# Optimization experiments

Measured on AMD Instinct MI355X. Metric: run time of the kernel, lower is better.

The kernel has to match this reference:

```python
import jax, jax.numpy as jnp
import numpy as np
from jax import lax

B, C, HW = 256, 3, 128
OC, K = 16, 3
NH, FANIN, NO = 256, 512, 10
F = OC * 63 * 63  # 63504 flattened features after conv(k=3,valid)->pool(2)


def setup_inputs() -> dict:
    key = jax.random.key(0)
    ks = jax.random.split(key, 8)
    inputs = jax.random.normal(ks[0], (B, C, HW, HW), dtype=jnp.float32)
    conv_w = jax.random.normal(ks[1], (OC, C, K, K), dtype=jnp.float32) * 0.1
    conv_b = jax.random.normal(ks[2], (OC,), dtype=jnp.float32) * 0.1
    hidden_idx = jax.random.randint(ks[3], (NH, FANIN), 0, F, dtype=jnp.int64 if jax.config.jax_enable_x64 else jnp.int32)
    hidden_w = jax.random.normal(ks[4], (NH, FANIN), dtype=jnp.float32) * (1.0 / np.sqrt(FANIN))
    hidden_b = jax.random.normal(ks[5], (NH,), dtype=jnp.float32) * 0.1
    out_w = jax.random.normal(ks[6], (NO, NH), dtype=jnp.float32) * (1.0 / np.sqrt(NH))
    out_b = jax.random.normal(ks[7], (NO,), dtype=jnp.float32) * 0.1
    return {"inputs": inputs, "conv_w": conv_w, "conv_b": conv_b,
            "hidden_idx": hidden_idx, "hidden_w": hidden_w, "hidden_b": hidden_b,
            "out_w": out_w, "out_b": out_b}


def reference(inputs, conv_w, conv_b, hidden_idx, hidden_w, hidden_b, out_w, out_b):
    # --- feature extraction: conv(valid) -> relu -> maxpool(2) -> flatten ---
    x = lax.conv_general_dilated(inputs, conv_w, window_strides=(1, 1), padding='VALID',
                                 dimension_numbers=('NCHW', 'OIHW', 'NCHW'))
    x = jax.nn.relu(x + conv_b[None, :, None, None])            # [B, OC, 126, 126]
    x = lax.reduce_window(x, -jnp.inf, lax.max,
                          window_dimensions=(1, 1, 2, 2),
                          window_strides=(1, 1, 2, 2), padding='VALID')  # [B, OC, 63, 63]
    feats = x.reshape(x.shape[0], -1)                           # [B, F] (row-major == torch.flatten)
    # --- NEAT-style classification: per-node gather -> tiny linear -> sigmoid ---
    gathered = feats[:, hidden_idx]                             # [B, NH, FANIN] irregular gather
    hidden = jax.nn.sigmoid(jnp.einsum('bhk,hk->bh', gathered, hidden_w) + hidden_b)  # [B, NH]
    out = jax.nn.sigmoid(hidden @ out_w.T + out_b)              # [B, NO]
    return out
```

## Files before the change

### kernel.cpp

```cpp
#include <hip/hip_runtime.h>
#include <hip/hip_fp16.h>
#include <math.h>

#define BATCH 256
#define CIN 3
#define HW 128
#define OC 16
#define POOLED 63
#define FEAT 63504
#define NH 256
#define FANIN 512
#define NO 10

#define PADX 134
#define ROWS 12

typedef _Float16 h4 __attribute__((ext_vector_type(4)));
typedef _Float16 h2v __attribute__((ext_vector_type(2)));
typedef float    f4 __attribute__((ext_vector_type(4)));

__global__ __launch_bounds__(256) void conv_pool_kernel(const float* __restrict__ inp,
                                                        const float* __restrict__ cw,
                                                        const float* __restrict__ cb,
                                                        __half* __restrict__ featsT) {
    __shared__ _Float16 sB[ROWS * 16 * PADX];
    const int t    = threadIdx.x;
    const int l    = t & 63;
    const int w    = t >> 6;
    const int q    = l >> 4;
    const int bcol = l & 15;

    const int id = blockIdx.x;
    const int u  = id & 7;
    const int v  = id >> 3;
    const int i  = v >> 1;
    const int g  = 2 * u + (v & 1);
    const int y0 = 2 * i;

#pragma unroll
    for (int bb = 0; bb < 4; ++bb) {
        const int b_l = w * 4 + bb;
#pragma unroll
        for (int rr = 0; rr < 12; ++rr) {
            const int c  = rr >> 2;
            const int dy = rr & 3;
            const float2 vv = *(const float2*)
                &inp[((size_t)(g * 16 + b_l) * CIN + c) * (HW * HW) + (y0 + dy) * HW + 2 * l];
            *(__half2*)&sB[(size_t)((c * 4 + dy) * 16 + b_l) * PADX + 2 * l] =
                __float22half2_rn(vv);
        }
    }
    __syncthreads();

    h4  aF[3][2];
    int bOff[3][2];
    float bias[4];
#pragma unroll
    for (int s = 0; s < 3; ++s) {
        const int rIdx = s * 4 + q;
        const int c    = (rIdx * 11) >> 5;
        const int ky   = rIdx - 3 * c;
        const bool valid = (c < 3);
        float wv[3];
#pragma unroll
        for (int kx = 0; kx < 3; ++kx)
            wv[kx] = valid ? cw[(bcol * CIN + c) * 9 + ky * 3 + kx] : 0.0f;
        aF[s][0][0] = (_Float16)wv[0]; aF[s][0][1] = (_Float16)wv[1];
        aF[s][0][2] = (_Float16)wv[2]; aF[s][0][3] = (_Float16)0.0f;
        aF[s][1][0] = (_Float16)0.0f;  aF[s][1][1] = (_Float16)wv[0];
        aF[s][1][2] = (_Float16)wv[1]; aF[s][1][3] = (_Float16)wv[2];
#pragma unroll
        for (int ys = 0; ys < 2; ++ys) {
            const int row = valid ? (c * 4 + ys + ky) : ys;
            bOff[s][ys] = (row * 16 + bcol) * PADX;
        }
    }
#pragma unroll
    for (int r = 0; r < 4; ++r) bias[r] = cb[4 * q + r];

    const int jend = (16 * w + 16 < 63) ? (16 * w + 16) : 63;
    for (int j = 16 * w; j < jend; ++j) {
        f4 d00 = {0.f,0.f,0.f,0.f}, d01 = d00, d10 = d00, d11 = d00;
#pragma unroll
        for (int s = 0; s < 3; ++s) {
            const _Float16* p0 = &sB[bOff[s][0] + 2 * j];
            const _Float16* p1 = &sB[bOff[s][1] + 2 * j];
            const h2v a0 = *(const h2v*)p0, a1 = *(const h2v*)(p0 + 2);
            const h2v c0 = *(const h2v*)p1, c1 = *(const h2v*)(p1 + 2);
            const h4 bF0 = {a0[0], a0[1], a1[0], a1[1]};
            const h4 bF1 = {c0[0], c0[1], c1[0], c1[1]};
            d00 = __builtin_amdgcn_mfma_f32_16x16x16f16(aF[s][0], bF0, d00, 0, 0, 0);
            d01 = __builtin_amdgcn_mfma_f32_16x16x16f16(aF[s][1], bF0, d01, 0, 0, 0);
            d10 = __builtin_amdgcn_mfma_f32_16x16x16f16(aF[s][0], bF1, d10, 0, 0, 0);
            d11 = __builtin_amdgcn_mfma_f32_16x16x16f16(aF[s][1], bF1, d11, 0, 0, 0);
        }
#pragma unroll
        for (int r = 0; r < 4; ++r) {
            const float mv = fmaxf(fmaxf(d00[r], d01[r]), fmaxf(d10[r], d11[r]));
            const float rv = fmaxf(mv + bias[r], 0.0f);
            const int oc = 4 * q + r;
            featsT[(size_t)(oc * 3969 + i * POOLED + j) * BATCH + g * 16 + bcol] =
                __float2half_rn(rv);
        }
    }
}

__global__ __launch_bounds__(256) void hidden_kernel(const __half* __restrict__ featsT,
                                                     const int* __restrict__ hidx,
                                                     const float* __restrict__ hw,
                                                     float* __restrict__ hiddenP) {
    __shared__ int   sidx[128];
    __shared__ float swt[128];
    __shared__ float red[4][256];
    const int h = blockIdx.x;
    const int q = blockIdx.y;
    const int t = threadIdx.x;
    if (t < 128) {
        sidx[t] = hidx[h * FANIN + q * 128 + t];
        swt[t]  = hw[h * FANIN + q * 128 + t];
    }
    __syncthreads();

    const int l   = t & 63;
    const int w   = t >> 6;
    const int hl  = l & 31;
    const int sel = l >> 5;
    float acc[8] = {0.f,0.f,0.f,0.f,0.f,0.f,0.f,0.f};
#pragma unroll
    for (int m = 0; m < 16; ++m) {
        const int kloc = w * 32 + 2 * m + sel;
        const uint4 v = *(const uint4*)(featsT + (size_t)sidx[kloc] * BATCH + 8 * hl);
        const __half2* hp = reinterpret_cast<const __half2*>(&v);
        const float wt = swt[kloc];
#pragma unroll
        for (int d2 = 0; d2 < 4; ++d2) {
            const float2 f = __half22float2(hp[d2]);
            acc[2 * d2 + 0] += f.x * wt;
            acc[2 * d2 + 1] += f.y * wt;
        }
    }
#pragma unroll
    for (int e = 0; e < 8; ++e) acc[e] += __shfl_xor(acc[e], 32);
    if (sel == 0) {
#pragma unroll
        for (int e = 0; e < 8; ++e) red[w][8 * hl + e] = acc[e];
    }
    __syncthreads();

    if (t < 256) {
        const float s = red[0][t] + red[1][t] + red[2][t] + red[3][t];
        hiddenP[((size_t)q * NH + h) * BATCH + t] = s;
    }
}

__global__ __launch_bounds__(256) void out_kernel(const float* __restrict__ hiddenP,
                                                  const float* __restrict__ hb,
                                                  const float* __restrict__ ow,
                                                  const float* __restrict__ ob,
                                                  float* __restrict__ out) {
    __shared__ float red[256];
    const int o  = blockIdx.x;
    const int bt = blockIdx.y;
    const int tb = threadIdx.x & 15;
    const int hg = threadIdx.x >> 4;
    const int b  = bt * 16 + tb;
    float acc = 0.f;
#pragma unroll
    for (int k = 0; k < 16; ++k) {
        const int h = hg * 16 + k;
        const float s = hiddenP[(0 * NH + h) * BATCH + b]
                      + hiddenP[(1 * NH + h) * BATCH + b]
                      + hiddenP[(2 * NH + h) * BATCH + b]
                      + hiddenP[(3 * NH + h) * BATCH + b] + hb[h];
        const float hs = 1.0f / (1.0f + __expf(-s));
        acc += hs * ow[o * NH + h];
    }
    red[threadIdx.x] = acc;
    __syncthreads();
    if (hg == 0) {
        float s = 0.f;
#pragma unroll
        for (int gg = 0; gg < 16; ++gg) s += red[gg * 16 + tb];
        out[b * NO + o] = 1.0f / (1.0f + __expf(-(s + ob[o])));
    }
}

extern "C" void kernel_launch(void* const* d_in, const int* in_sizes, int n_in,
                              void* d_out, int out_size, void* d_ws, size_t ws_size,
                              hipStream_t stream) {
    const float* inputs   = (const float*)d_in[0];
    const float* conv_w   = (const float*)d_in[1];
    const float* conv_b   = (const float*)d_in[2];
    const int*   hidden_i = (const int*)d_in[3];
    const float* hidden_w = (const float*)d_in[4];
    const float* hidden_b = (const float*)d_in[5];
    const float* out_w    = (const float*)d_in[6];
    const float* out_b    = (const float*)d_in[7];
    float* out = (float*)d_out;

    char* ws = (char*)d_ws;
    __half* featsT  = (__half*)ws;
    float*  hiddenP = (float*)(ws + (size_t)FEAT * BATCH * 2);

    conv_pool_kernel<<<1008, 256, 0, stream>>>(inputs, conv_w, conv_b, featsT);
    hidden_kernel<<<dim3(NH, 4), 256, 0, stream>>>(featsT, hidden_i, hidden_w, hiddenP);
    out_kernel<<<dim3(NO, 16), 256, 0, stream>>>(hiddenP, hidden_b, out_w, out_b, out);
}
```

Before: 135.0 us.

## Restructure hidden gather kernel: per-block batch slice, full fan-in, fused sigmoid

The hidden-layer kernel now gives each block a 32-sample batch slice and 8 hidden nodes, and each node covers its full 512-element fan-in, reduced across lanes with shuffles. The old split into four fan-in partials is gone. Bias and sigmoid are applied in the hidden kernel, so the output kernel reads one finished activation instead of summing four partial buffers. This removes the partial-sum traffic and the shared-memory reduction. In exchange, the gather reads only 64-byte segments per feature row instead of 512 bytes, and index and weight loads are repeated across the 8 batch-slice blocks.

```diff
diff --git a/kernel.cpp b/kernel.cpp
--- a/kernel.cpp
+++ b/kernel.cpp
@@ -108,53 +108,61 @@
 __global__ __launch_bounds__(256) void hidden_kernel(const __half* __restrict__ featsT,
                                                      const int* __restrict__ hidx,
                                                      const float* __restrict__ hw,
-                                                     float* __restrict__ hiddenP) {
-    __shared__ int   sidx[128];
-    __shared__ float swt[128];
-    __shared__ float red[4][256];
-    const int h = blockIdx.x;
-    const int q = blockIdx.y;
-    const int t = threadIdx.x;
-    if (t < 128) {
-        sidx[t] = hidx[h * FANIN + q * 128 + t];
-        swt[t]  = hw[h * FANIN + q * 128 + t];
-    }
-    __syncthreads();
-
+                                                     const float* __restrict__ hb,
+                                                     float* __restrict__ hiddenT) {
+    const int id  = blockIdx.x;
+    const int u   = id & 7;
+    const int seg = id >> 3;
+    const int t   = threadIdx.x;
+    const int w   = t >> 6;
     const int l   = t & 63;
-    const int w   = t >> 6;
-    const int hl  = l & 31;
-    const int sel = l >> 5;
-    float acc[8] = {0.f,0.f,0.f,0.f,0.f,0.f,0.f,0.f};
-#pragma unroll
-    for (int m = 0; m < 16; ++m) {
-        const int kloc = w * 32 + 2 * m + sel;
-        const uint4 v = *(const uint4*)(featsT + (size_t)sidx[kloc] * BATCH + 8 * hl);
-        const __half2* hp = reinterpret_cast<const __half2*>(&v);
-        const float wt = swt[kloc];
-#pragma unroll
-        for (int d2 = 0; d2 < 4; ++d2) {
-            const float2 f = __half22float2(hp[d2]);
-            acc[2 * d2 + 0] += f.x * wt;
-            acc[2 * d2 + 1] += f.y * wt;
-        }
-    }
-#pragma unroll
-    for (int e = 0; e < 8; ++e) acc[e] += __shfl_xor(acc[e], 32);
-    if (sel == 0) {
-#pragma unroll
-        for (int e = 0; e < 8; ++e) red[w][8 * hl + e] = acc[e];
-    }
-    __syncthreads();
-
-    if (t < 256) {
-        const float s = red[0][t] + red[1][t] + red[2][t] + red[3][t];
-        hiddenP[((size_t)q * NH + h) * BATCH + t] = s;
-    }
-}
-
-__global__ __launch_bounds__(256) void out_kernel(const float* __restrict__ hiddenP,
-                                                  const float* __restrict__ hb,
+    const int rg  = l >> 2;
+    const int bq  = l & 3;
+
+#pragma unroll 1
+    for (int hh = 0; hh < 2; ++hh) {
+        const int h = seg * 8 + w * 2 + hh;
+        float acc[8] = {0.f,0.f,0.f,0.f,0.f,0.f,0.f,0.f};
+#pragma unroll 8
+        for (int m = 0; m < 32; ++m) {
+            const int kk  = m * 16 + rg;
+            const int row = hidx[h * FANIN + kk];
+            const float wt = hw[h * FANIN + kk];
+            const uint4 v = *(const uint4*)(featsT + (size_t)row * BATCH + u * 32 + bq * 8);
+            const __half2* hp = reinterpret_cast<const __half2*>(&v);
+#pragma unroll
+            for (int d2 = 0; d2 < 4; ++d2) {
+                const float2 f = __half22float2(hp[d2]);
+                acc[2 * d2 + 0] += f.x * wt;
+                acc[2 * d2 + 1] += f.y * wt;
+            }
+        }
+#pragma unroll
+        for (int e = 0; e < 8; ++e) {
+            acc[e] += __shfl_xor(acc[e], 4);
+            acc[e] += __shfl_xor(acc[e], 8);
+            acc[e] += __shfl_xor(acc[e], 16);
+            acc[e] += __shfl_xor(acc[e], 32);
+        }
+        if (rg == 0) {
+            const float bias = hb[h];
+            float4 o0, o1;
+            o0.x = 1.f / (1.f + __expf(-(acc[0] + bias)));
+            o0.y = 1.f / (1.f + __expf(-(acc[1] + bias)));
+            o0.z = 1.f / (1.f + __expf(-(acc[2] + bias)));
+            o0.w = 1.f / (1.f + __expf(-(acc[3] + bias)));
+            o1.x = 1.f / (1.f + __expf(-(acc[4] + bias)));
+            o1.y = 1.f / (1.f + __expf(-(acc[5] + bias)));
+            o1.z = 1.f / (1.f + __expf(-(acc[6] + bias)));
+            o1.w = 1.f / (1.f + __expf(-(acc[7] + bias)));
+            float* dst = &hiddenT[h * BATCH + u * 32 + bq * 8];
+            *(float4*)dst       = o0;
+            *(float4*)(dst + 4) = o1;
+        }
+    }
+}
+
+__global__ __launch_bounds__(256) void out_kernel(const float* __restrict__ hiddenT,
                                                   const float* __restrict__ ow,
                                                   const float* __restrict__ ob,
                                                   float* __restrict__ out) {
@@ -168,19 +176,14 @@
 #pragma unroll
     for (int k = 0; k < 16; ++k) {
         const int h = hg * 16 + k;
-        const float s = hiddenP[(0 * NH + h) * BATCH + b]
-                      + hiddenP[(1 * NH + h) * BATCH + b]
-                      + hiddenP[(2 * NH + h) * BATCH + b]
-                      + hiddenP[(3 * NH + h) * BATCH + b] + hb[h];
-        const float hs = 1.0f / (1.0f + __expf(-s));
-        acc += hs * ow[o * NH + h];
+        acc += hiddenT[h * BATCH + b] * ow[o * NH + h];
     }
     red[threadIdx.x] = acc;
     __syncthreads();
     if (hg == 0) {
         float s = 0.f;
 #pragma unroll
-        for (int gg = 0; gg < 16; ++gg) s += red[gg * 16 + tb];
+        for (int g = 0; g < 16; ++g) s += red[g * 16 + tb];
         out[b * NO + o] = 1.0f / (1.0f + __expf(-(s + ob[o])));
     }
 }
@@ -200,9 +203,9 @@
 
     char* ws = (char*)d_ws;
     __half* featsT  = (__half*)ws;
-    float*  hiddenP = (float*)(ws + (size_t)FEAT * BATCH * 2);
+    float*  hiddenT = (float*)(ws + (size_t)FEAT * BATCH * 2);
 
     conv_pool_kernel<<<1008, 256, 0, stream>>>(inputs, conv_w, conv_b, featsT);
-    hidden_kernel<<<dim3(NH, 4), 256, 0, stream>>>(featsT, hidden_i, hidden_w, hiddenP);
-    out_kernel<<<dim3(NO, 16), 256, 0, stream>>>(hiddenP, hidden_b, out_w, out_b, out);
-}
+    hidden_kernel<<<256, 256, 0, stream>>>(featsT, hidden_i, hidden_w, hidden_b, hiddenT);
+    out_kernel<<<dim3(NO, 16), 256, 0, stream>>>(hiddenT, out_w, out_b, out);
+}
```

Measured after the change: 140.7 us. 4.2% more time.

## Fuse conv, hidden and output stages into one persistent kernel with grid barriers

Applied to the files above, without the earlier changes.

Merges the three kernel launches into a single persistent kernel of 512 blocks. Blocks loop over conv tiles, then over hidden units, and finally compute the output layer. The stages are separated by atomic-counter grid barriers, and the counter is cleared with a memset before launch. This removes launch gaps and tail effects between kernels, but adds barrier spin cost and a co-residency requirement. Conv tiles also become unevenly distributed across blocks (126 or 2 per 8 blocks).

```diff
diff --git a/kernel.cpp b/kernel.cpp
--- a/kernel.cpp
+++ b/kernel.cpp
@@ -14,174 +14,205 @@
 
 #define PADX 134
 #define ROWS 12
+#define SMEM_BYTES (ROWS * 16 * PADX * 2)
+#define NBLK 512u
 
 typedef _Float16 h4 __attribute__((ext_vector_type(4)));
 typedef _Float16 h2v __attribute__((ext_vector_type(2)));
 typedef float    f4 __attribute__((ext_vector_type(4)));
 
-__global__ __launch_bounds__(256) void conv_pool_kernel(const float* __restrict__ inp,
-                                                        const float* __restrict__ cw,
-                                                        const float* __restrict__ cb,
-                                                        __half* __restrict__ featsT) {
-    __shared__ _Float16 sB[ROWS * 16 * PADX];
-    const int t    = threadIdx.x;
-    const int l    = t & 63;
-    const int w    = t >> 6;
-    const int q    = l >> 4;
-    const int bcol = l & 15;
-
-    const int id = blockIdx.x;
-    const int u  = id & 7;
-    const int v  = id >> 3;
-    const int i  = v >> 1;
-    const int g  = 2 * u + (v & 1);
-    const int y0 = 2 * i;
-
-#pragma unroll
-    for (int bb = 0; bb < 4; ++bb) {
-        const int b_l = w * 4 + bb;
-#pragma unroll
-        for (int rr = 0; rr < 12; ++rr) {
-            const int c  = rr >> 2;
-            const int dy = rr & 3;
-            const float2 vv = *(const float2*)
-                &inp[((size_t)(g * 16 + b_l) * CIN + c) * (HW * HW) + (y0 + dy) * HW + 2 * l];
-            *(__half2*)&sB[(size_t)((c * 4 + dy) * 16 + b_l) * PADX + 2 * l] =
-                __float22half2_rn(vv);
-        }
-    }
+__device__ __forceinline__ void grid_barrier(unsigned* cnt) {
     __syncthreads();
-
-    h4  aF[3][2];
-    int bOff[3][2];
-    float bias[4];
-#pragma unroll
-    for (int s = 0; s < 3; ++s) {
-        const int rIdx = s * 4 + q;
-        const int c    = (rIdx * 11) >> 5;
-        const int ky   = rIdx - 3 * c;
-        const bool valid = (c < 3);
-        float wv[3];
-#pragma unroll
-        for (int kx = 0; kx < 3; ++kx)
-            wv[kx] = valid ? cw[(bcol * CIN + c) * 9 + ky * 3 + kx] : 0.0f;
-        aF[s][0][0] = (_Float16)wv[0]; aF[s][0][1] = (_Float16)wv[1];
-        aF[s][0][2] = (_Float16)wv[2]; aF[s][0][3] = (_Float16)0.0f;
-        aF[s][1][0] = (_Float16)0.0f;  aF[s][1][1] = (_Float16)wv[0];
-        aF[s][1][2] = (_Float16)wv[1]; aF[s][1][3] = (_Float16)wv[2];
-#pragma unroll
-        for (int ys = 0; ys < 2; ++ys) {
-            const int row = valid ? (c * 4 + ys + ky) : ys;
-            bOff[s][ys] = (row * 16 + bcol) * PADX;
-        }
-    }
-#pragma unroll
-    for (int r = 0; r < 4; ++r) bias[r] = cb[4 * q + r];
-
-    const int jend = (16 * w + 16 < 63) ? (16 * w + 16) : 63;
-    for (int j = 16 * w; j < jend; ++j) {
-        f4 d00 = {0.f,0.f,0.f,0.f}, d01 = d00, d10 = d00, d11 = d00;
+    if (threadIdx.x == 0) {
+        __threadfence();
+        atomicAdd(cnt, 1u);
+        while (__hip_atomic_load(cnt, __ATOMIC_ACQUIRE, __HIP_MEMORY_SCOPE_AGENT) < NBLK) {
+            __builtin_amdgcn_s_sleep(8);
+        }
+    }
+    __syncthreads();
+}
+
+__global__ __launch_bounds__(256) void fused_kernel(const float* __restrict__ inp,
+                                                    const float* __restrict__ cw,
+                                                    const float* __restrict__ cb,
+                                                    const int* __restrict__ hidx,
+                                                    const float* __restrict__ hw,
+                                                    const float* __restrict__ hb,
+                                                    const float* __restrict__ ow,
+                                                    const float* __restrict__ ob,
+                                                    __half* __restrict__ featsT,
+                                                    float* __restrict__ hiddenP,
+                                                    unsigned* __restrict__ bar,
+                                                    float* __restrict__ out) {
+    __shared__ __align__(16) char smem[SMEM_BYTES];
+    const int bid = blockIdx.x;
+    const int t   = threadIdx.x;
+
+    {
+        _Float16* sB = (_Float16*)smem;
+        const int l    = t & 63;
+        const int w    = t >> 6;
+        const int q    = l >> 4;
+        const int bcol = l & 15;
+        const int u    = bid & 7;
+
+        h4  aF[3][2];
+        int bOff[3][2];
+        float bias[4];
 #pragma unroll
         for (int s = 0; s < 3; ++s) {
-            const _Float16* p0 = &sB[bOff[s][0] + 2 * j];
-            const _Float16* p1 = &sB[bOff[s][1] + 2 * j];
-            const h2v a0 = *(const h2v*)p0, a1 = *(const h2v*)(p0 + 2);
-            const h2v c0 = *(const h2v*)p1, c1 = *(const h2v*)(p1 + 2);
-            const h4 bF0 = {a0[0], a0[1], a1[0], a1[1]};
-            const h4 bF1 = {c0[0], c0[1], c1[0], c1[1]};
-            d00 = __builtin_amdgcn_mfma_f32_16x16x16f16(aF[s][0], bF0, d00, 0, 0, 0);
-            d01 = __builtin_amdgcn_mfma_f32_16x16x16f16(aF[s][1], bF0, d01, 0, 0, 0);
-            d10 = __builtin_amdgcn_mfma_f32_16x16x16f16(aF[s][0], bF1, d10, 0, 0, 0);
-            d11 = __builtin_amdgcn_mfma_f32_16x16x16f16(aF[s][1], bF1, d11, 0, 0, 0);
-        }
-#pragma unroll
-        for (int r = 0; r < 4; ++r) {
-            const float mv = fmaxf(fmaxf(d00[r], d01[r]), fmaxf(d10[r], d11[r]));
-            const float rv = fmaxf(mv + bias[r], 0.0f);
-            const int oc = 4 * q + r;
-            featsT[(size_t)(oc * 3969 + i * POOLED + j) * BATCH + g * 16 + bcol] =
-                __float2half_rn(rv);
-        }
-    }
-}
-
-__global__ __launch_bounds__(256) void hidden_kernel(const __half* __restrict__ featsT,
-                                                     const int* __restrict__ hidx,
-                                                     const float* __restrict__ hw,
-                                                     float* __restrict__ hiddenP) {
-    __shared__ int   sidx[128];
-    __shared__ float swt[128];
-    __shared__ float red[4][256];
-    const int h = blockIdx.x;
-    const int q = blockIdx.y;
-    const int t = threadIdx.x;
-    if (t < 128) {
-        sidx[t] = hidx[h * FANIN + q * 128 + t];
-        swt[t]  = hw[h * FANIN + q * 128 + t];
-    }
-    __syncthreads();
-
-    const int l   = t & 63;
-    const int w   = t >> 6;
-    const int hl  = l & 31;
-    const int sel = l >> 5;
-    float acc[8] = {0.f,0.f,0.f,0.f,0.f,0.f,0.f,0.f};
-#pragma unroll
-    for (int m = 0; m < 16; ++m) {
-        const int kloc = w * 32 + 2 * m + sel;
-        const uint4 v = *(const uint4*)(featsT + (size_t)sidx[kloc] * BATCH + 8 * hl);
-        const __half2* hp = reinterpret_cast<const __half2*>(&v);
-        const float wt = swt[kloc];
-#pragma unroll
-        for (int d2 = 0; d2 < 4; ++d2) {
-            const float2 f = __half22float2(hp[d2]);
-            acc[2 * d2 + 0] += f.x * wt;
-            acc[2 * d2 + 1] += f.y * wt;
-        }
-    }
-#pragma unroll
-    for (int e = 0; e < 8; ++e) acc[e] += __shfl_xor(acc[e], 32);
-    if (sel == 0) {
-#pragma unroll
-        for (int e = 0; e < 8; ++e) red[w][8 * hl + e] = acc[e];
-    }
-    __syncthreads();
-
-    if (t < 256) {
-        const float s = red[0][t] + red[1][t] + red[2][t] + red[3][t];
-        hiddenP[((size_t)q * NH + h) * BATCH + t] = s;
-    }
-}
-
-__global__ __launch_bounds__(256) void out_kernel(const float* __restrict__ hiddenP,
-                                                  const float* __restrict__ hb,
-                                                  const float* __restrict__ ow,
-                                                  const float* __restrict__ ob,
-                                                  float* __restrict__ out) {
-    __shared__ float red[256];
-    const int o  = blockIdx.x;
-    const int bt = blockIdx.y;
-    const int tb = threadIdx.x & 15;
-    const int hg = threadIdx.x >> 4;
-    const int b  = bt * 16 + tb;
-    float acc = 0.f;
-#pragma unroll
-    for (int k = 0; k < 16; ++k) {
-        const int h = hg * 16 + k;
-        const float s = hiddenP[(0 * NH + h) * BATCH + b]
-                      + hiddenP[(1 * NH + h) * BATCH + b]
-                      + hiddenP[(2 * NH + h) * BATCH + b]
-                      + hiddenP[(3 * NH + h) * BATCH + b] + hb[h];
-        const float hs = 1.0f / (1.0f + __expf(-s));
-        acc += hs * ow[o * NH + h];
-    }
-    red[threadIdx.x] = acc;
-    __syncthreads();
-    if (hg == 0) {
-        float s = 0.f;
-#pragma unroll
-        for (int gg = 0; gg < 16; ++gg) s += red[gg * 16 + tb];
-        out[b * NO + o] = 1.0f / (1.0f + __expf(-(s + ob[o])));
+            const int rIdx = s * 4 + q;
+            const int c    = (rIdx * 11) >> 5;
+            const int ky   = rIdx - 3 * c;
+            const bool valid = (c < 3);
+            float wv[3];
+#pragma unroll
+            for (int kx = 0; kx < 3; ++kx)
+                wv[kx] = valid ? cw[(bcol * CIN + c) * 9 + ky * 3 + kx] : 0.0f;
+            aF[s][0][0] = (_Float16)wv[0]; aF[s][0][1] = (_Float16)wv[1];
+            aF[s][0][2] = (_Float16)wv[2]; aF[s][0][3] = (_Float16)0.0f;
+            aF[s][1][0] = (_Float16)0.0f;  aF[s][1][1] = (_Float16)wv[0];
+            aF[s][1][2] = (_Float16)wv[1]; aF[s][1][3] = (_Float16)wv[2];
+#pragma unroll
+            for (int ys = 0; ys < 2; ++ys) {
+                const int row = valid ? (c * 4 + ys + ky) : ys;
+                bOff[s][ys] = (row * 16 + bcol) * PADX;
+            }
+        }
+#pragma unroll
+        for (int r = 0; r < 4; ++r) bias[r] = cb[4 * q + r];
+
+#pragma unroll 1
+        for (int tt = bid >> 3; tt < 126; tt += 64) {
+            const int i  = tt >> 1;
+            const int g  = 2 * u + (tt & 1);
+            const int y0 = 2 * i;
+
+            __syncthreads();
+#pragma unroll
+            for (int bb = 0; bb < 4; ++bb) {
+                const int b_l = w * 4 + bb;
+#pragma unroll
+                for (int rr = 0; rr < 12; ++rr) {
+                    const int c  = rr >> 2;
+                    const int dy = rr & 3;
+                    const float2 vv = *(const float2*)
+                        &inp[((size_t)(g * 16 + b_l) * CIN + c) * (HW * HW) + (y0 + dy) * HW + 2 * l];
+                    *(__half2*)&sB[(size_t)((c * 4 + dy) * 16 + b_l) * PADX + 2 * l] =
+                        __float22half2_rn(vv);
+                }
+            }
+            __syncthreads();
+
+            const int jend = (16 * w + 16 < 63) ? (16 * w + 16) : 63;
+            for (int j = 16 * w; j < jend; ++j) {
+                f4 d00 = {0.f,0.f,0.f,0.f}, d01 = d00, d10 = d00, d11 = d00;
+#pragma unroll
+                for (int s = 0; s < 3; ++s) {
+                    const _Float16* p0 = &sB[bOff[s][0] + 2 * j];
+                    const _Float16* p1 = &sB[bOff[s][1] + 2 * j];
+                    const h2v a0 = *(const h2v*)p0, a1 = *(const h2v*)(p0 + 2);
+                    const h2v c0 = *(const h2v*)p1, c1 = *(const h2v*)(p1 + 2);
+                    const h4 bF0 = {a0[0], a0[1], a1[0], a1[1]};
+                    const h4 bF1 = {c0[0], c0[1], c1[0], c1[1]};
+                    d00 = __builtin_amdgcn_mfma_f32_16x16x16f16(aF[s][0], bF0, d00, 0, 0, 0);
+                    d01 = __builtin_amdgcn_mfma_f32_16x16x16f16(aF[s][1], bF0, d01, 0, 0, 0);
+                    d10 = __builtin_amdgcn_mfma_f32_16x16x16f16(aF[s][0], bF1, d10, 0, 0, 0);
+                    d11 = __builtin_amdgcn_mfma_f32_16x16x16f16(aF[s][1], bF1, d11, 0, 0, 0);
+                }
+#pragma unroll
+                for (int r = 0; r < 4; ++r) {
+                    const float mv = fmaxf(fmaxf(d00[r], d01[r]), fmaxf(d10[r], d11[r]));
+                    const float rv = fmaxf(mv + bias[r], 0.0f);
+                    const int oc = 4 * q + r;
+                    featsT[(size_t)(oc * 3969 + i * POOLED + j) * BATCH + g * 16 + bcol] =
+                        __float2half_rn(rv);
+                }
+            }
+        }
+    }
+
+    grid_barrier(&bar[0]);
+
+    {
+        int*   sidx = (int*)smem;
+        float* swt  = (float*)(smem + 512);
+        float (*red)[256] = (float (*)[256])(smem + 1024);
+        const int l   = t & 63;
+        const int w   = t >> 6;
+        const int hl  = l & 31;
+        const int sel = l >> 5;
+
+#pragma unroll 1
+        for (int unit = bid; unit < 1024; unit += NBLK) {
+            const int h = unit & 255;
+            const int q = unit >> 8;
+            __syncthreads();
+            if (t < 128) {
+                sidx[t] = hidx[h * FANIN + q * 128 + t];
+                swt[t]  = hw[h * FANIN + q * 128 + t];
+            }
+            __syncthreads();
+
+            float acc[8] = {0.f,0.f,0.f,0.f,0.f,0.f,0.f,0.f};
+#pragma unroll
+            for (int m = 0; m < 16; ++m) {
+                const int kloc = w * 32 + 2 * m + sel;
+                const uint4 v = *(const uint4*)(featsT + (size_t)sidx[kloc] * BATCH + 8 * hl);
+                const __half2* hp = reinterpret_cast<const __half2*>(&v);
+                const float wt = swt[kloc];
+#pragma unroll
+                for (int d2 = 0; d2 < 4; ++d2) {
+                    const float2 f = __half22float2(hp[d2]);
+                    acc[2 * d2 + 0] += f.x * wt;
+                    acc[2 * d2 + 1] += f.y * wt;
+                }
+            }
+#pragma unroll
+            for (int e = 0; e < 8; ++e) acc[e] += __shfl_xor(acc[e], 32);
+            if (sel == 0) {
+#pragma unroll
+                for (int e = 0; e < 8; ++e) red[w][8 * hl + e] = acc[e];
+            }
+            __syncthreads();
+
+            if (t < 256) {
+                const float s = red[0][t] + red[1][t] + red[2][t] + red[3][t];
+                hiddenP[((size_t)q * NH + h) * BATCH + t] = s;
+            }
+        }
+    }
+
+    grid_barrier(&bar[1]);
+
+    if (bid < 160) {
+        float* red = (float*)smem;
+        const int o  = bid >> 4;
+        const int bt = bid & 15;
+        const int tb = t & 15;
+        const int hg = t >> 4;
+        const int b  = bt * 16 + tb;
+        float acc = 0.f;
+#pragma unroll
+        for (int k = 0; k < 16; ++k) {
+            const int h = hg * 16 + k;
+            const float s = hiddenP[(0 * NH + h) * BATCH + b]
+                          + hiddenP[(1 * NH + h) * BATCH + b]
+                          + hiddenP[(2 * NH + h) * BATCH + b]
+                          + hiddenP[(3 * NH + h) * BATCH + b] + hb[h];
+            const float hs = 1.0f / (1.0f + __expf(-s));
+            acc += hs * ow[o * NH + h];
+        }
+        __syncthreads();
+        red[t] = acc;
+        __syncthreads();
+        if (hg == 0) {
+            float s = 0.f;
+#pragma unroll
+            for (int gg = 0; gg < 16; ++gg) s += red[gg * 16 + tb];
+            out[b * NO + o] = 1.0f / (1.0f + __expf(-(s + ob[o])));
+        }
     }
 }
 
@@ -199,10 +230,15 @@
     float* out = (float*)d_out;
 
     char* ws = (char*)d_ws;
-    __half* featsT  = (__half*)ws;
-    float*  hiddenP = (float*)(ws + (size_t)FEAT * BATCH * 2);
-
-    conv_pool_kernel<<<1008, 256, 0, stream>>>(inputs, conv_w, conv_b, featsT);
-    hidden_kernel<<<dim3(NH, 4), 256, 0, stream>>>(featsT, hidden_i, hidden_w, hiddenP);
-    out_kernel<<<dim3(NO, 16), 256, 0, stream>>>(hiddenP, hidden_b, out_w, out_b, out);
+    __half*   featsT  = (__half*)ws;
+    float*    hiddenP = (float*)(ws + (size_t)FEAT * BATCH * 2);
+    unsigned* bar     = (unsigned*)(ws + (size_t)FEAT * BATCH * 2
+                                       + (size_t)4 * NH * BATCH * 4);
+
+    hipMemsetAsync(bar, 0, 64, stream);
+
+    fused_kernel<<<NBLK, 256, 0, stream>>>(inputs, conv_w, conv_b,
+                                           hidden_i, hidden_w, hidden_b,
+                                           out_w, out_b,
+                                           featsT, hiddenP, bar, out);
 }
```

Result: slower. 270.5 us (+100.4%).

## Fuse output layer into hidden kernel via last-block atomic counter

Applied to the files above, without the earlier changes.

Merges the hidden and output kernels into one launch. Every block bumps a global atomic counter, and the last block to finish computes the sigmoid hidden activations and the 10-way output layer for all 256 batch rows. This removes one kernel launch and its gap, but adds a memset launch. The whole output-layer computation, 256 hidden units times 10 outputs per batch row, now runs serially in a single block.

```diff
diff --git a/kernel.cpp b/kernel.cpp
--- a/kernel.cpp
+++ b/kernel.cpp
@@ -105,16 +105,23 @@
     }
 }
 
-__global__ __launch_bounds__(256) void hidden_kernel(const __half* __restrict__ featsT,
-                                                     const int* __restrict__ hidx,
-                                                     const float* __restrict__ hw,
-                                                     float* __restrict__ hiddenP) {
+__global__ __launch_bounds__(256) void hidden_out_kernel(const __half* __restrict__ featsT,
+                                                         const int* __restrict__ hidx,
+                                                         const float* __restrict__ hw,
+                                                         const float* __restrict__ hb,
+                                                         const float* __restrict__ ow,
+                                                         const float* __restrict__ ob,
+                                                         float* __restrict__ hiddenP,
+                                                         unsigned* __restrict__ cnt,
+                                                         float* __restrict__ out) {
     __shared__ int   sidx[128];
     __shared__ float swt[128];
     __shared__ float red[4][256];
-    const int h = blockIdx.x;
-    const int q = blockIdx.y;
-    const int t = threadIdx.x;
+    __shared__ int   lastFlag;
+    const int bid = blockIdx.x;
+    const int h   = bid & 255;
+    const int q   = bid >> 8;
+    const int t   = threadIdx.x;
     if (t < 128) {
         sidx[t] = hidx[h * FANIN + q * 128 + t];
         swt[t]  = hw[h * FANIN + q * 128 + t];
@@ -151,38 +158,39 @@
         const float s = red[0][t] + red[1][t] + red[2][t] + red[3][t];
         hiddenP[((size_t)q * NH + h) * BATCH + t] = s;
     }
-}
-
-__global__ __launch_bounds__(256) void out_kernel(const float* __restrict__ hiddenP,
-                                                  const float* __restrict__ hb,
-                                                  const float* __restrict__ ow,
-                                                  const float* __restrict__ ob,
-                                                  float* __restrict__ out) {
-    __shared__ float red[256];
-    const int o  = blockIdx.x;
-    const int bt = blockIdx.y;
-    const int tb = threadIdx.x & 15;
-    const int hg = threadIdx.x >> 4;
-    const int b  = bt * 16 + tb;
-    float acc = 0.f;
-#pragma unroll
-    for (int k = 0; k < 16; ++k) {
-        const int h = hg * 16 + k;
-        const float s = hiddenP[(0 * NH + h) * BATCH + b]
-                      + hiddenP[(1 * NH + h) * BATCH + b]
-                      + hiddenP[(2 * NH + h) * BATCH + b]
-                      + hiddenP[(3 * NH + h) * BATCH + b] + hb[h];
+
+    __syncthreads();
+    if (t == 0) {
+        __threadfence();
+        const unsigned old = __hip_atomic_fetch_add(cnt, 1u, __ATOMIC_RELAXED,
+                                                    __HIP_MEMORY_SCOPE_AGENT);
+        if (old == 1023u) {
+            (void)__hip_atomic_load(cnt, __ATOMIC_ACQUIRE, __HIP_MEMORY_SCOPE_AGENT);
+            lastFlag = 1;
+        } else {
+            lastFlag = 0;
+        }
+    }
+    __syncthreads();
+    if (!lastFlag) return;
+
+    const int b = t;
+    float oacc[NO];
+#pragma unroll
+    for (int o = 0; o < NO; ++o) oacc[o] = 0.f;
+#pragma unroll 4
+    for (int hh = 0; hh < NH; ++hh) {
+        const float s = hiddenP[(0 * NH + hh) * BATCH + b]
+                      + hiddenP[(1 * NH + hh) * BATCH + b]
+                      + hiddenP[(2 * NH + hh) * BATCH + b]
+                      + hiddenP[(3 * NH + hh) * BATCH + b] + hb[hh];
         const float hs = 1.0f / (1.0f + __expf(-s));
-        acc += hs * ow[o * NH + h];
-    }
-    red[threadIdx.x] = acc;
-    __syncthreads();
-    if (hg == 0) {
-        float s = 0.f;
-#pragma unroll
-        for (int gg = 0; gg < 16; ++gg) s += red[gg * 16 + tb];
-        out[b * NO + o] = 1.0f / (1.0f + __expf(-(s + ob[o])));
-    }
+#pragma unroll
+        for (int o = 0; o < NO; ++o) oacc[o] += hs * ow[o * NH + hh];
+    }
+#pragma unroll
+    for (int o = 0; o < NO; ++o)
+        out[b * NO + o] = 1.0f / (1.0f + __expf(-(oacc[o] + ob[o])));
 }
 
 extern "C" void kernel_launch(void* const* d_in, const int* in_sizes, int n_in,
@@ -199,10 +207,14 @@
     float* out = (float*)d_out;
 
     char* ws = (char*)d_ws;
-    __half* featsT  = (__half*)ws;
-    float*  hiddenP = (float*)(ws + (size_t)FEAT * BATCH * 2);
+    __half*   featsT  = (__half*)ws;
+    float*    hiddenP = (float*)(ws + (size_t)FEAT * BATCH * 2);
+    unsigned* cnt     = (unsigned*)(ws + (size_t)FEAT * BATCH * 2
+                                       + (size_t)4 * NH * BATCH * 4);
+
+    hipMemsetAsync(cnt, 0, 64, stream);
 
     conv_pool_kernel<<<1008, 256, 0, stream>>>(inputs, conv_w, conv_b, featsT);
-    hidden_kernel<<<dim3(NH, 4), 256, 0, stream>>>(featsT, hidden_i, hidden_w, hiddenP);
-    out_kernel<<<dim3(NO, 16), 256, 0, stream>>>(hiddenP, hidden_b, out_w, out_b, out);
+    hidden_out_kernel<<<1024, 256, 0, stream>>>(featsT, hidden_i, hidden_w, hidden_b,
+                                                out_w, out_b, hiddenP, cnt, out);
 }
```

After: 195.1 us. +44.5%, slower.
